# Optimization experiments

Hardware: AMD Instinct MI355X
Metric: run time of the kernel (lower is better)

## Reference

```python
import jax, jax.numpy as jnp
import numpy as np

B, S, ID = 4, 1024, 4096
R, RP, H, D = 512, 64, 32, 128  # lora_rank, rope_dim, n_heads, head_dim
EPS = 1.1920929e-07  # torch nn.RMSNorm default eps = finfo(float32).eps


def rms_norm(x, w):
    return x * jax.lax.rsqrt(jnp.mean(x * x, axis=-1, keepdims=True) + EPS) * w


def rope(x, cos_half, sin_half):
    # half/half pairing rotation (HF style)
    cos = jnp.concatenate([cos_half, cos_half], axis=-1)
    sin = jnp.concatenate([sin_half, sin_half], axis=-1)
    half = x.shape[-1] // 2
    rot = jnp.concatenate([-x[..., half:], x[..., :half]], axis=-1)
    return x * cos + rot * sin


def setup_inputs() -> dict:
    key = jax.random.key(0)
    ks = jax.random.split(key, 12)
    sc = 0.02
    x = jax.random.normal(ks[0], (B, S, ID), jnp.float32)
    # real RoPE tables, shape (S, RP//2)
    inv_freq = 1.0 / (10000.0 ** (jnp.arange(0, RP, 2, dtype=jnp.float32) / RP))
    ang = jnp.arange(S, dtype=jnp.float32)[:, None] * inv_freq[None, :]
    cos_half = jnp.cos(ang)
    sin_half = jnp.sin(ang)
    mask = jnp.zeros((S, S), jnp.float32)  # additive mask; no softmax in module so keep finite
    return {
        "x": x,
        "cos_half": cos_half,
        "sin_half": sin_half,
        "mask": mask,
        "w_dkv_kr_w": jax.random.normal(ks[1], (R + RP, ID), jnp.float32) * sc,
        "w_dkv_kr_b": jnp.zeros((R + RP,), jnp.float32),
        "kv_norm_w": jnp.ones((R,), jnp.float32),
        "w_dq_w": jax.random.normal(ks[2], (R, ID), jnp.float32) * sc,
        "w_dq_b": jnp.zeros((R,), jnp.float32),
        "q_norm_w": jnp.ones((R,), jnp.float32),
        "w_uq_w": jax.random.normal(ks[3], (H * D, R), jnp.float32) * sc,
        "w_uq_b": jnp.zeros((H * D,), jnp.float32),
        "w_qr_w": jax.random.normal(ks[4], (RP, R), jnp.float32) * sc,
        "w_qr_b": jnp.zeros((RP,), jnp.float32),
        "w_uk_w": jax.random.normal(ks[5], (H * D, R), jnp.float32) * sc,
        "w_uv_w": jax.random.normal(ks[6], (H * D, R), jnp.float32) * sc,
        "w_o_w": jax.random.normal(ks[7], (ID, H * D), jnp.float32) * sc,
        "w_o_b": jnp.zeros((ID,), jnp.float32),
        "start_pos": 0,
    }


def reference(x, cos_half, sin_half, mask, w_dkv_kr_w, w_dkv_kr_b, kv_norm_w,
              w_dq_w, w_dq_b, q_norm_w, w_uq_w, w_uq_b, w_qr_w, w_qr_b,
              w_uk_w, w_uv_w, w_o_w, w_o_b, start_pos):
    b, s, _ = x.shape
    # KV down-projection + decoupled rope key
    dkv = x @ w_dkv_kr_w.T + w_dkv_kr_b                      # (b,s,R+RP)
    c_kv = rms_norm(dkv[..., :R], kv_norm_w)                 # (b,s,R) == kv_cache[:,start:end] (start_pos=0, prefill)
    k_r = rope(dkv[..., R:], cos_half, sin_half)             # (b,s,RP) == pe_cache slice
    # Q path
    c_q = rms_norm(x @ w_dq_w.T + w_dq_b, q_norm_w)          # (b,s,R)
    q = (c_q @ w_uq_w.T + w_uq_b).reshape(b, s, H, D)        # (b,s,h,d)
    q_r = rope(c_q @ w_qr_w.T + w_qr_b, cos_half, sin_half)  # (b,s,RP)
    # weight absorption: fold w_uk into the query
    qW = jnp.einsum('bshd,hdr->bshr', q, w_uk_w.reshape(H, D, R))
    scores = jnp.einsum('bshr,btr->bsht', qW, c_kv)
    scores = scores + jnp.einsum('bsd,btd->bst', q_r, k_r)[:, :, None, :]
    scores = scores + mask[:, None, :]                       # (s,1,t) broadcast over (b,s,h,t)
    # NOTE: faithful to source -- no softmax / no scaling applied
    a_sum = jnp.einsum('bsht,btr->bshr', scores, c_kv)
    out = jnp.einsum('bshr,hdr->bshd', a_sum, w_uv_w.reshape(H, D, R))
    out = out.reshape(b, s, H * D)
    return out @ w_o_w.T + w_o_b
```

## Files before the change

### kernel.cpp

```cpp
#include <hip/hip_runtime.h>
#include <hip/hip_bf16.h>

typedef __attribute__((ext_vector_type(8))) short s8v;
typedef __attribute__((ext_vector_type(4))) float f4v;
typedef __hip_bfloat16 bf16;

#define BSZ 4
#define SEQ 1024
#define IDIM 4096
#define RNK 512
#define RPD 64
#define NH 32
#define HD 128
#define BT 4096

__device__ __forceinline__ void load_lds16(const bf16* g, bf16* l) {
  __builtin_amdgcn_global_load_lds((const __attribute__((address_space(1))) void*)g,
                                   (__attribute__((address_space(3))) void*)l, 16, 0, 0);
}

template<int OUT_BF16, int HAS_BIAS>
__global__ __launch_bounds__(512, 2) void gemm256(
    const bf16* __restrict__ A, const bf16* __restrict__ B, void* __restrict__ Cv,
    const float* __restrict__ bias, int K, int lda, int ldb, int ldc, int NXT)
{
  __shared__ bf16 As[2][256 * 64];
  __shared__ bf16 Bs[2][256 * 64];

  int nwg = gridDim.x, orig = blockIdx.x, cpx = nwg >> 3;
  int l = (orig & 7) * cpx + (orig >> 3);
  int tx = l % NXT, ty = l / NXT;
  long long rowBase = (long long)ty * 256;
  long long colBase = (long long)tx * 256;

  int tid = threadIdx.x, lane = tid & 63, wave = tid >> 6;
  int wr = wave >> 2, wc = wave & 3;
  int lrow = lane & 15, lslot = lane >> 4;
  int NT = K >> 6;

  int srow = tid >> 3, sslot = tid & 7;
  int skc = sslot ^ (srow & 7);
  int sdst = srow * 64 + sslot * 8;
  const bf16* aP0 = A + (rowBase + srow      ) * lda + (skc << 3);
  const bf16* aP1 = A + (rowBase + srow +  64) * lda + (skc << 3);
  const bf16* aP2 = A + (rowBase + srow + 128) * lda + (skc << 3);
  const bf16* aP3 = A + (rowBase + srow + 192) * lda + (skc << 3);
  const bf16* bP0 = B + (colBase + srow      ) * ldb + (skc << 3);
  const bf16* bP1 = B + (colBase + srow +  64) * ldb + (skc << 3);
  const bf16* bP2 = B + (colBase + srow + 128) * ldb + (skc << 3);
  const bf16* bP3 = B + (colBase + srow + 192) * ldb + (skc << 3);

#define SG_A(bs, dk, i) load_lds16(aP##i + (dk) * 64, &As[bs][sdst + (i) * 4096])
#define SG_B(bs, dk, i) load_lds16(bP##i + (dk) * 64, &Bs[bs][sdst + (i) * 4096])

  int offk0 = ((lslot ^ (lrow & 7)) << 3);
  int offk1 = (((4 | lslot) ^ (lrow & 7)) << 3);
  int aoff = (wr * 128 + lrow) * 64;
  int boff = (wc * 64 + lrow) * 64;

  f4v acc[8][4];
  #pragma unroll
  for (int m = 0; m < 8; ++m)
    #pragma unroll
    for (int n = 0; n < 4; ++n) acc[m][n] = {0.f, 0.f, 0.f, 0.f};

#define PHASE(BSEL, Q, STG, GATE) do {                                         \
    const bf16* Ab_ = &As[BSEL][aoff];                                         \
    s8v a00 = *(const s8v*)(Ab_ + (2*(Q))   * 1024 + offk0);                   \
    s8v a01 = *(const s8v*)(Ab_ + (2*(Q))   * 1024 + offk1);                   \
    s8v a10 = *(const s8v*)(Ab_ + (2*(Q)+1) * 1024 + offk0);                   \
    s8v a11 = *(const s8v*)(Ab_ + (2*(Q)+1) * 1024 + offk1);                   \
    if ((Q) == 0) {                                                            \
      const bf16* Bb_ = &Bs[BSEL][boff];                                       \
      _Pragma("unroll")                                                        \
      for (int n = 0; n < 4; ++n) {                                            \
        b0[n] = *(const s8v*)(Bb_ + n * 1024 + offk0);                         \
        b1[n] = *(const s8v*)(Bb_ + n * 1024 + offk1);                         \
      }                                                                        \
    }                                                                          \
    STG;                                                                       \
    if ((Q) == 0) asm volatile("s_waitcnt lgkmcnt(8)");                        \
    __builtin_amdgcn_s_barrier();                                              \
    __builtin_amdgcn_s_setprio(1);                                             \
    _Pragma("unroll")                                                          \
    for (int n = 0; n < 4; ++n)                                                \
      acc[2*(Q)][n]   = __builtin_amdgcn_mfma_f32_16x16x32_bf16(a00, b0[n], acc[2*(Q)][n], 0, 0, 0);   \
    _Pragma("unroll")                                                          \
    for (int n = 0; n < 4; ++n)                                                \
      acc[2*(Q)+1][n] = __builtin_amdgcn_mfma_f32_16x16x32_bf16(a10, b0[n], acc[2*(Q)+1][n], 0, 0, 0); \
    _Pragma("unroll")                                                          \
    for (int n = 0; n < 4; ++n)                                                \
      acc[2*(Q)][n]   = __builtin_amdgcn_mfma_f32_16x16x32_bf16(a01, b1[n], acc[2*(Q)][n], 0, 0, 0);   \
    _Pragma("unroll")                                                          \
    for (int n = 0; n < 4; ++n)                                                \
      acc[2*(Q)+1][n] = __builtin_amdgcn_mfma_f32_16x16x32_bf16(a11, b1[n], acc[2*(Q)+1][n], 0, 0, 0); \
    __builtin_amdgcn_s_setprio(0);                                             \
    GATE;                                                                      \
    __builtin_amdgcn_s_barrier();                                              \
  } while (0)

  SG_A(0, 0, 0); SG_A(0, 0, 1); SG_A(0, 0, 2); SG_A(0, 0, 3);
  SG_B(0, 0, 0); SG_B(0, 0, 1); SG_B(0, 0, 2); SG_B(0, 0, 3);
  SG_B(1, 1, 0); SG_B(1, 1, 1); SG_B(1, 1, 2); SG_B(1, 1, 3);
  asm volatile("s_waitcnt vmcnt(4)" ::: "memory");
  __builtin_amdgcn_s_barrier();

  for (int u = 0; u < NT; u += 2) {
    bool st = (u + 2 < NT);
    s8v b0[4], b1[4];
    PHASE(0, 0, { SG_A(1, 1, 0); SG_A(1, 1, 1); }, {});
    PHASE(0, 1, { SG_A(1, 1, 2); SG_A(1, 1, 3); }, {});
    PHASE(0, 2, { if (st) { SG_B(0, 2, 0); SG_B(0, 2, 1); } }, {});
    PHASE(0, 3, { if (st) { SG_B(0, 2, 2); SG_B(0, 2, 3); } },
          { if (st) asm volatile("s_waitcnt vmcnt(4)" ::: "memory");
            else    asm volatile("s_waitcnt vmcnt(0)" ::: "memory"); });
    PHASE(1, 0, { if (st) { SG_A(0, 2, 0); SG_A(0, 2, 1); } }, {});
    PHASE(1, 1, { if (st) { SG_A(0, 2, 2); SG_A(0, 2, 3); } }, {});
    PHASE(1, 2, { if (st) { SG_B(1, 3, 0); SG_B(1, 3, 1); } }, {});
    PHASE(1, 3, { if (st) { SG_B(1, 3, 2); SG_B(1, 3, 3); } },
          { if (st) asm volatile("s_waitcnt vmcnt(4)" ::: "memory"); });
    aP0 += 128; aP1 += 128; aP2 += 128; aP3 += 128;
    bP0 += 128; bP1 += 128; bP2 += 128; bP3 += 128;
  }
#undef PHASE
#undef SG_A
#undef SG_B

  float* Cf = (float*)Cv;
  bf16* Cb = (bf16*)Cv;
  int lcol = lane & 15, lr4 = (lane >> 4) * 4;
  #pragma unroll
  for (int m = 0; m < 8; ++m)
    #pragma unroll
    for (int n = 0; n < 4; ++n) {
      long long col = colBase + wc * 64 + n * 16 + lcol;
      float bv_ = HAS_BIAS ? bias[col] : 0.f;
      #pragma unroll
      for (int j = 0; j < 4; ++j) {
        long long row = rowBase + wr * 128 + m * 16 + lr4 + j;
        float v = acc[m][n][j] + bv_;
        if (OUT_BF16) Cb[row * ldc + col] = __float2bfloat16(v);
        else          Cf[row * ldc + col] = v;
      }
    }
}

template<int BM, int BN, int WTM, int WTN, int OUT_BF16, int ADD_MODE, int HAS_BIAS>
__global__ __launch_bounds__(256) void gemm_bt(
    const bf16* __restrict__ A, const bf16* __restrict__ B, void* __restrict__ Cv,
    const float* __restrict__ bias, const void* __restrict__ addend,
    int K, int lda, int ldb, int ldc, int ldadd, int nz2,
    long long sA1, long long sA2, long long sB1, long long sB2,
    long long sC1, long long sC2, long long sD1, long long sD2)
{
  constexpr int BK = 32;
  constexpr int WM = BM / WTM, WN = BN / WTN;
  constexpr int FM = WM / 16, FN = WN / 16;
  static_assert(WTM * WTN == 4, "4 waves / 256 threads");
  static_assert((BM * BK) % 2048 == 0 && (BN * BK) % 2048 == 0, "staging coverage");
  __shared__ alignas(16) bf16 As[BM * BK];
  __shared__ alignas(16) bf16 Bs[BN * BK];

  int z = blockIdx.z;
  int z1 = z / nz2, z2 = z - z1 * nz2;
  A += z1 * sA1 + z2 * sA2;
  B += z1 * sB1 + z2 * sB2;
  long long coff = z1 * sC1 + z2 * sC2;
  long long doffz = z1 * sD1 + z2 * sD2;

  int tid = threadIdx.x;
  int lane = tid & 63, wave = tid >> 6;
  int wr = wave / WTN, wc = wave % WTN;
  int rowBase = blockIdx.y * BM;
  int colBase = blockIdx.x * BN;

  f4v acc[FM][FN];
  #pragma unroll
  for (int i = 0; i < FM; ++i)
    #pragma unroll
    for (int j = 0; j < FN; ++j) acc[i][j] = {0.f, 0.f, 0.f, 0.f};

  constexpr int A_LOADS = (BM * BK) / 2048;
  constexpr int B_LOADS = (BN * BK) / 2048;
  int lrow = lane & 15;
  int rsw = (lrow >> 1) & 3;
  int lkA = ((lane >> 4) ^ rsw) * 8;

  for (int k0 = 0; k0 < K; k0 += BK) {
    #pragma unroll
    for (int i = 0; i < A_LOADS; ++i) {
      int e = tid * 8 + i * 2048;
      int r_ = e >> 5, sp_ = (e >> 3) & 3, kc_ = sp_ ^ ((r_ >> 1) & 3);
      load_lds16(A + (long long)(rowBase + r_) * lda + k0 + (kc_ << 3), &As[e]);
    }
    #pragma unroll
    for (int i = 0; i < B_LOADS; ++i) {
      int e = tid * 8 + i * 2048;
      int r_ = e >> 5, sp_ = (e >> 3) & 3, kc_ = sp_ ^ ((r_ >> 1) & 3);
      load_lds16(B + (long long)(colBase + r_) * ldb + k0 + (kc_ << 3), &Bs[e]);
    }
    __syncthreads();

    s8v av[FM], bv[FN];
    #pragma unroll
    for (int fm = 0; fm < FM; ++fm)
      av[fm] = *(const s8v*)&As[(wr * WM + fm * 16 + lrow) * BK + lkA];
    #pragma unroll
    for (int fn = 0; fn < FN; ++fn)
      bv[fn] = *(const s8v*)&Bs[(wc * WN + fn * 16 + lrow) * BK + lkA];
    #pragma unroll
    for (int fm = 0; fm < FM; ++fm)
      #pragma unroll
      for (int fn = 0; fn < FN; ++fn)
        acc[fm][fn] = __builtin_amdgcn_mfma_f32_16x16x32_bf16(av[fm], bv[fn], acc[fm][fn], 0, 0, 0);
    __syncthreads();
  }

  bf16* Cb = (bf16*)Cv;
  float* Cf = (float*)Cv;
  const float* addf = (const float*)addend;
  const bf16* addb = (const bf16*)addend;
  int lcol = lane & 15, lr4 = (lane >> 4) * 4;
  #pragma unroll
  for (int fm = 0; fm < FM; ++fm) {
    #pragma unroll
    for (int fn = 0; fn < FN; ++fn) {
      int col = colBase + wc * WN + fn * 16 + lcol;
      #pragma unroll
      for (int j = 0; j < 4; ++j) {
        int row = rowBase + wr * WM + fm * 16 + lr4 + j;
        float v = acc[fm][fn][j];
        if (HAS_BIAS) v += bias[col];
        if (ADD_MODE == 1) v += addf[doffz + (long long)row * ldadd + col];
        if (ADD_MODE == 2) v += __bfloat162float(addb[doffz + (long long)row * ldadd + col]);
        long long idx = coff + (long long)row * ldc + col;
        if (OUT_BF16) Cb[idx] = __float2bfloat16(v);
        else          Cf[idx] = v;
      }
    }
  }
}


__global__ void cast4(const float* __restrict__ in, bf16* __restrict__ out, int n4) {
  int i = blockIdx.x * 256 + threadIdx.x;
  if (i >= n4) return;
  float4 v = ((const float4*)in)[i];
  union { ushort4 u; bf16 h[4]; } o;
  o.h[0] = __float2bfloat16(v.x); o.h[1] = __float2bfloat16(v.y);
  o.h[2] = __float2bfloat16(v.z); o.h[3] = __float2bfloat16(v.w);
  ((ushort4*)out)[i] = o.u;
}

struct CastJobs {
  const float* s[8];
  bf16* d[8];
  int n4[8];
  int b0[8];
};
__global__ __launch_bounds__(256) void cast_multi(CastJobs J) {
  int blk = blockIdx.x, j = 0;
  #pragma unroll
  for (int k = 1; k < 8; ++k) if (blk >= J.b0[k]) j = k;
  int i = (blk - J.b0[j]) * 256 + threadIdx.x;
  if (i >= J.n4[j]) return;
  float4 v = ((const float4*)J.s[j])[i];
  union { ushort4 u; bf16 h[4]; } o;
  o.h[0] = __float2bfloat16(v.x); o.h[1] = __float2bfloat16(v.y);
  o.h[2] = __float2bfloat16(v.z); o.h[3] = __float2bfloat16(v.w);
  ((ushort4*)J.d[j])[i] = o.u;
}

__global__ __launch_bounds__(256) void tr_bf16(const bf16* __restrict__ in, bf16* __restrict__ out,
                                               int R, int C) {
  __shared__ bf16 t[32][33];
  long long zo = (long long)blockIdx.z * R * C;
  int c0 = blockIdx.x * 32, r0 = blockIdx.y * 32;
  int tx = threadIdx.x & 31, ty = threadIdx.x >> 5;
  #pragma unroll
  for (int i = 0; i < 32; i += 8)
    t[ty + i][tx] = in[zo + (long long)(r0 + ty + i) * C + (c0 + tx)];
  __syncthreads();
  #pragma unroll
  for (int i = 0; i < 32; i += 8)
    out[zo + (long long)(c0 + ty + i) * R + (r0 + tx)] = t[tx][ty + i];
}

__device__ __forceinline__ float block_sum256(float v) {
  #pragma unroll
  for (int o = 32; o > 0; o >>= 1) v += __shfl_xor(v, o, 64);
  __shared__ float red[4];
  int lane = threadIdx.x & 63, w = threadIdx.x >> 6;
  if (lane == 0) red[w] = v;
  __syncthreads();
  return red[0] + red[1] + red[2] + red[3];
}

__global__ __launch_bounds__(256) void rms_dkv(const float* __restrict__ dq,
    const float* __restrict__ w, const float* __restrict__ ch, const float* __restrict__ sh,
    bf16* __restrict__ ckv, bf16* __restrict__ kr) {
  int row = blockIdx.x, t = threadIdx.x;
  const float* xr = dq + (long long)row * 1088;
  float v0 = xr[t], v1 = xr[t + 256];
  float ss = block_sum256(v0 * v0 + v1 * v1);
  float sc = rsqrtf(ss * (1.0f / 512.0f) + 1.1920929e-07f);
  long long o = (long long)row * 512;
  ckv[o + t]       = __float2bfloat16(v0 * sc * w[t]);
  ckv[o + t + 256] = __float2bfloat16(v1 * sc * w[t + 256]);
  if (t < 64) {
    int s = row & (SEQ - 1);
    float a = xr[512 + t], r;
    if (t < 32) r = a * ch[s * 32 + t]      - xr[512 + t + 32] * sh[s * 32 + t];
    else        r = a * ch[s * 32 + t - 32] + xr[512 + t - 32] * sh[s * 32 + t - 32];
    kr[(long long)row * 64 + t] = __float2bfloat16(r);
  }
}

__global__ __launch_bounds__(256) void rms512(const float* __restrict__ dq,
    const float* __restrict__ w, bf16* __restrict__ out) {
  int row = blockIdx.x, t = threadIdx.x;
  const float* xr = dq + (long long)row * 1088 + 576;
  float v0 = xr[t], v1 = xr[t + 256];
  float ss = block_sum256(v0 * v0 + v1 * v1);
  float sc = rsqrtf(ss * (1.0f / 512.0f) + 1.1920929e-07f);
  long long o = (long long)row * 512;
  out[o + t]       = __float2bfloat16(v0 * sc * w[t]);
  out[o + t + 256] = __float2bfloat16(v1 * sc * w[t + 256]);
}

__global__ void rope_qr(const float* __restrict__ in, const float* __restrict__ ch,
                        const float* __restrict__ sh, bf16* __restrict__ out) {
  int row = blockIdx.x, t = threadIdx.x;
  const float* xr = in + (long long)row * 64;
  int s = row & (SEQ - 1);
  float a = xr[t], r;
  if (t < 32) r = a * ch[s * 32 + t]      - xr[t + 32] * sh[s * 32 + t];
  else        r = a * ch[s * 32 + t - 32] + xr[t - 32] * sh[s * 32 + t - 32];
  out[(long long)row * 64 + t] = __float2bfloat16(r);
}

extern "C" void kernel_launch(void* const* d_in, const int* in_sizes, int n_in,
                              void* d_out, int out_size, void* d_ws, size_t ws_size,
                              hipStream_t stream) {
  const float* x    = (const float*)d_in[0];
  const float* ch   = (const float*)d_in[1];
  const float* sh   = (const float*)d_in[2];
  const float* mask = (const float*)d_in[3];
  const float* wdkv = (const float*)d_in[4];
  const float* bdkv = (const float*)d_in[5];
  const float* kvnw = (const float*)d_in[6];
  const float* wdq  = (const float*)d_in[7];
  const float* bdq  = (const float*)d_in[8];
  const float* qnw  = (const float*)d_in[9];
  const float* wuq  = (const float*)d_in[10];
  const float* buq  = (const float*)d_in[11];
  const float* wqr  = (const float*)d_in[12];
  const float* bqr  = (const float*)d_in[13];
  const float* wuk  = (const float*)d_in[14];
  const float* wuv  = (const float*)d_in[15];
  const float* wo   = (const float*)d_in[16];
  const float* bo   = (const float*)d_in[17];
  float* out = (float*)d_out;
  (void)in_sizes; (void)n_in; (void)out_size; (void)ws_size;

  char* ws = (char*)d_ws;
  bf16* regionA = (bf16*)(ws);
  bf16* outh    = (bf16*)(ws + 33554432);
  bf16* wdkv_b  = (bf16*)(ws + 67108864);
  bf16* wdq_b   = (bf16*)(ws + 71827456);
  bf16* wuq_b   = (bf16*)(ws + 76021760);
  bf16* wqr_b   = (bf16*)(ws + 80216064);
  bf16* wuv_b   = (bf16*)(ws + 80281600);
  bf16* wuk_b   = (bf16*)(ws + 84475904);
  bf16* mask_b  = (bf16*)(ws + 88670208);
  char* regionB = ws + 90767360;
  float* dq_cat = (float*)(regionB);
  bf16* Eb      = (bf16*)(regionB);
  bf16* FT      = (bf16*)(regionB + 16777216);

  bf16* xb   = regionA;
  bf16* wo_b = regionA;

  char* ob = (char*)d_out;
  bf16* qb     = (bf16*)(ob);
  char* U      = ob + 33554432;
  bf16* ckv    = (bf16*)(U);
  bf16* kr     = (bf16*)(U + 4194304);
  bf16* ckvT   = (bf16*)(U + 4718592);
  bf16* krT    = (bf16*)(U + 8912896);
  bf16* cq     = (bf16*)(U + 9437184);
  float* qr_pre= (float*)(U + 13631488);
  bf16* qr_b   = (bf16*)(U + 14680064);
  bf16* Gm     = (bf16*)(U + 15204352);
  bf16* Mt     = (bf16*)(U + 17301504);
  bf16* base_b = (bf16*)(U + 17563648);

  float* bias_cat = qr_pre;

  long long Z = 0;

  {
    CastJobs J;
    const float* srcs[8] = {x, wdkv, wdq, wqr, mask, wuq, wuv, wuk};
    bf16* dsts[8] = {xb, wdkv_b, wdq_b, wqr_b, mask_b, wuq_b, wuv_b, wuk_b};
    int n4s[8] = {4194304, 589824, 524288, 8192, 262144, 524288, 524288, 524288};
    int accb = 0;
    for (int j = 0; j < 8; ++j) {
      J.s[j] = srcs[j]; J.d[j] = dsts[j]; J.n4[j] = n4s[j];
      J.b0[j] = accb; accb += (n4s[j] + 255) / 256;
    }
    cast_multi<<<dim3(accb), 256, 0, stream>>>(J);
  }
  hipMemcpyAsync(bias_cat, bdkv, 576 * 4, hipMemcpyDeviceToDevice, stream);
  hipMemcpyAsync(bias_cat + 576, bdq, 512 * 4, hipMemcpyDeviceToDevice, stream);

  gemm_bt<128, 64, 4, 1, 0, 0, 1><<<dim3(17, 32, 1), 256, 0, stream>>>(
      xb, wdkv_b, dq_cat, bias_cat, nullptr, 4096, 4096, 4096, 1088, 0, 1, Z,Z,Z,Z,Z,Z,Z,Z);
  rms_dkv<<<dim3(BT), 256, 0, stream>>>(dq_cat, kvnw, ch, sh, ckv, kr);
  rms512<<<dim3(BT), 256, 0, stream>>>(dq_cat, qnw, cq);
  tr_bf16<<<dim3(16, 32, 4), 256, 0, stream>>>(ckv, ckvT, 1024, 512);
  tr_bf16<<<dim3(2, 32, 4), 256, 0, stream>>>(kr, krT, 1024, 64);

  cast4<<<dim3(16384), 256, 0, stream>>>(wo, wo_b, 4194304);

  gemm256<1, 1><<<dim3(256), 512, 0, stream>>>(
      cq, wuq_b, qb, buq, 512, 512, 512, 4096, 16);

  gemm_bt<128, 64, 4, 1, 0, 0, 1><<<dim3(1, 32, 1), 256, 0, stream>>>(
      cq, wqr_b, qr_pre, bqr, nullptr, 512, 512, 512, 64, 0, 1, Z,Z,Z,Z,Z,Z,Z,Z);
  rope_qr<<<dim3(BT), 64, 0, stream>>>(qr_pre, ch, sh, qr_b);

  gemm_bt<128, 128, 2, 2, 1, 0, 0><<<dim3(4, 4, 4), 256, 0, stream>>>(
      ckvT, ckvT, Gm, nullptr, nullptr, 1024, 1024, 1024, 512, 0, 1,
      524288LL, Z, 524288LL, Z, 262144LL, Z, Z, Z);

  gemm_bt<128, 64, 4, 1, 1, 0, 0><<<dim3(1, 4, 4), 256, 0, stream>>>(
      ckvT, krT, Mt, nullptr, nullptr, 1024, 1024, 1024, 64, 0, 1,
      524288LL, Z, 65536LL, Z, 32768LL, Z, Z, Z);

  gemm_bt<128, 128, 2, 2, 1, 0, 0><<<dim3(4, 8, 4), 256, 0, stream>>>(
      mask_b, ckvT, base_b, nullptr, nullptr, 1024, 1024, 1024, 512, 0, 1,
      Z, Z, 524288LL, Z, 524288LL, Z, Z, Z);

  gemm_bt<128, 128, 2, 2, 1, 2, 0><<<dim3(4, 8, 4), 256, 0, stream>>>(
      qr_b, Mt, base_b, nullptr, base_b, 64, 64, 64, 512, 512, 1,
      65536LL, Z, 32768LL, Z, 524288LL, Z, 524288LL, Z);

  gemm256<1, 0><<<dim3(256), 512, 0, stream>>>(
      base_b, wuv_b, outh, nullptr, 512, 512, 512, 4096, 16);

  gemm_bt<128, 128, 2, 2, 1, 0, 0><<<dim3(4, 1, 128), 256, 0, stream>>>(
      wuv_b, Gm, Eb, nullptr, nullptr, 512, 512, 512, 512, 0, 32,
      Z, 65536LL, 262144LL, Z, 2097152LL, 65536LL, Z, Z);

  gemm_bt<128, 128, 2, 2, 1, 0, 0><<<dim3(1, 1, 128), 256, 0, stream>>>(
      Eb, wuk_b, FT, nullptr, nullptr, 512, 512, 512, 128, 0, 32,
      2097152LL, 65536LL, Z, 65536LL, 524288LL, 16384LL, Z, Z);

  gemm_bt<128, 128, 2, 2, 1, 2, 0><<<dim3(1, 8, 128), 256, 0, stream>>>(
      qb, FT, outh, nullptr, outh, 128, 4096, 128, 4096, 4096, 32,
      4194304LL, 128LL, 524288LL, 16384LL, 4194304LL, 128LL, 4194304LL, 128LL);

  gemm256<0, 1><<<dim3(256), 512, 0, stream>>>(
      outh, wo_b, out, bo, 4096, 4096, 4096, 4096, 16);
}
```

Baseline: 458.9 us.

## Halve K-tile depth and software-pipeline LDS fragment reads across MFMA phases

The 256x256 GEMM now stages K=32 slices instead of 64, which halves shared memory per buffer. It changes the swizzle and staging layout and prefetches the next A/B register fragments while the current MFMAs run. Launch bounds drop to one block per SIMD-pair hint so the extra prefetch registers fit. This is meant to hide LDS read latency behind matrix math, at the cost of twice as many barriers per unit of K and possibly lower occupancy.

```diff
diff --git a/kernel.cpp b/kernel.cpp
--- a/kernel.cpp
+++ b/kernel.cpp
@@ -20,12 +20,12 @@
 }
 
 template<int OUT_BF16, int HAS_BIAS>
-__global__ __launch_bounds__(512, 2) void gemm256(
+__global__ __launch_bounds__(512, 1) void gemm256(
     const bf16* __restrict__ A, const bf16* __restrict__ B, void* __restrict__ Cv,
     const float* __restrict__ bias, int K, int lda, int ldb, int ldc, int NXT)
 {
-  __shared__ bf16 As[2][256 * 64];
-  __shared__ bf16 Bs[2][256 * 64];
+  __shared__ bf16 As[2][256 * 32];
+  __shared__ bf16 Bs[2][256 * 32];
 
   int nwg = gridDim.x, orig = blockIdx.x, cpx = nwg >> 3;
   int l = (orig & 7) * cpx + (orig >> 3);
@@ -36,27 +36,29 @@
   int tid = threadIdx.x, lane = tid & 63, wave = tid >> 6;
   int wr = wave >> 2, wc = wave & 3;
   int lrow = lane & 15, lslot = lane >> 4;
-  int NT = K >> 6;
-
-  int srow = tid >> 3, sslot = tid & 7;
-  int skc = sslot ^ (srow & 7);
-  int sdst = srow * 64 + sslot * 8;
-  const bf16* aP0 = A + (rowBase + srow      ) * lda + (skc << 3);
-  const bf16* aP1 = A + (rowBase + srow +  64) * lda + (skc << 3);
-  const bf16* aP2 = A + (rowBase + srow + 128) * lda + (skc << 3);
-  const bf16* aP3 = A + (rowBase + srow + 192) * lda + (skc << 3);
-  const bf16* bP0 = B + (colBase + srow      ) * ldb + (skc << 3);
-  const bf16* bP1 = B + (colBase + srow +  64) * ldb + (skc << 3);
-  const bf16* bP2 = B + (colBase + srow + 128) * ldb + (skc << 3);
-  const bf16* bP3 = B + (colBase + srow + 192) * ldb + (skc << 3);
-
-#define SG_A(bs, dk, i) load_lds16(aP##i + (dk) * 64, &As[bs][sdst + (i) * 4096])
-#define SG_B(bs, dk, i) load_lds16(bP##i + (dk) * 64, &Bs[bs][sdst + (i) * 4096])
-
-  int offk0 = ((lslot ^ (lrow & 7)) << 3);
-  int offk1 = (((4 | lslot) ^ (lrow & 7)) << 3);
-  int aoff = (wr * 128 + lrow) * 64;
-  int boff = (wc * 64 + lrow) * 64;
+  int NT = K >> 5;
+
+  int r0 = tid >> 2, sp = tid & 3;
+  int kc0 = sp ^ ((r0 >> 1) & 3);
+  const bf16* aQ0 = A + (rowBase + r0      ) * lda + kc0 * 8;
+  const bf16* aQ1 = A + (rowBase + r0 + 128) * lda + kc0 * 8;
+  const bf16* bQ0 = B + (colBase + r0      ) * ldb + kc0 * 8;
+  const bf16* bQ1 = B + (colBase + r0 + 128) * ldb + kc0 * 8;
+  int sdst = tid * 8;
+
+#define SGA(bs, dk, h) load_lds16((h ? aQ1 : aQ0) + (dk) * 32, &As[bs][sdst + (h) * 4096])
+#define SGB(bs, dk, h) load_lds16((h ? bQ1 : bQ0) + (dk) * 32, &Bs[bs][sdst + (h) * 4096])
+
+  int kOff = (lslot ^ ((lrow >> 1) & 3)) * 8;
+  int aBase = (wr * 128 + lrow) * 32 + kOff;
+  int bBase = (wc * 64 + lrow) * 32 + kOff;
+
+#define RD_A(d0, d1, bs, m) do { \
+    d0 = *(const s8v*)&As[bs][aBase + (m) * 512]; \
+    d1 = *(const s8v*)&As[bs][aBase + ((m) + 1) * 512]; } while (0)
+#define RD_B(arr, bs) do { \
+    _Pragma("unroll") \
+    for (int n_ = 0; n_ < 4; ++n_) arr[n_] = *(const s8v*)&Bs[bs][bBase + n_ * 512]; } while (0)
 
   f4v acc[8][4];
   #pragma unroll
@@ -64,67 +66,73 @@
     #pragma unroll
     for (int n = 0; n < 4; ++n) acc[m][n] = {0.f, 0.f, 0.f, 0.f};
 
-#define PHASE(BSEL, Q, STG, GATE) do {                                         \
-    const bf16* Ab_ = &As[BSEL][aoff];                                         \
-    s8v a00 = *(const s8v*)(Ab_ + (2*(Q))   * 1024 + offk0);                   \
-    s8v a01 = *(const s8v*)(Ab_ + (2*(Q))   * 1024 + offk1);                   \
-    s8v a10 = *(const s8v*)(Ab_ + (2*(Q)+1) * 1024 + offk0);                   \
-    s8v a11 = *(const s8v*)(Ab_ + (2*(Q)+1) * 1024 + offk1);                   \
-    if ((Q) == 0) {                                                            \
-      const bf16* Bb_ = &Bs[BSEL][boff];                                       \
-      _Pragma("unroll")                                                        \
-      for (int n = 0; n < 4; ++n) {                                            \
-        b0[n] = *(const s8v*)(Bb_ + n * 1024 + offk0);                         \
-        b1[n] = *(const s8v*)(Bb_ + n * 1024 + offk1);                         \
-      }                                                                        \
-    }                                                                          \
-    STG;                                                                       \
-    if ((Q) == 0) asm volatile("s_waitcnt lgkmcnt(8)");                        \
-    __builtin_amdgcn_s_barrier();                                              \
-    __builtin_amdgcn_s_setprio(1);                                             \
-    _Pragma("unroll")                                                          \
-    for (int n = 0; n < 4; ++n)                                                \
-      acc[2*(Q)][n]   = __builtin_amdgcn_mfma_f32_16x16x32_bf16(a00, b0[n], acc[2*(Q)][n], 0, 0, 0);   \
-    _Pragma("unroll")                                                          \
-    for (int n = 0; n < 4; ++n)                                                \
-      acc[2*(Q)+1][n] = __builtin_amdgcn_mfma_f32_16x16x32_bf16(a10, b0[n], acc[2*(Q)+1][n], 0, 0, 0); \
-    _Pragma("unroll")                                                          \
-    for (int n = 0; n < 4; ++n)                                                \
-      acc[2*(Q)][n]   = __builtin_amdgcn_mfma_f32_16x16x32_bf16(a01, b1[n], acc[2*(Q)][n], 0, 0, 0);   \
-    _Pragma("unroll")                                                          \
-    for (int n = 0; n < 4; ++n)                                                \
-      acc[2*(Q)+1][n] = __builtin_amdgcn_mfma_f32_16x16x32_bf16(a11, b1[n], acc[2*(Q)+1][n], 0, 0, 0); \
-    __builtin_amdgcn_s_setprio(0);                                             \
-    GATE;                                                                      \
-    __builtin_amdgcn_s_barrier();                                              \
-  } while (0)
-
-  SG_A(0, 0, 0); SG_A(0, 0, 1); SG_A(0, 0, 2); SG_A(0, 0, 3);
-  SG_B(0, 0, 0); SG_B(0, 0, 1); SG_B(0, 0, 2); SG_B(0, 0, 3);
-  SG_B(1, 1, 0); SG_B(1, 1, 1); SG_B(1, 1, 2); SG_B(1, 1, 3);
-  asm volatile("s_waitcnt vmcnt(4)" ::: "memory");
+#define MMP(mp, A0, A1, BB) do { \
+    __builtin_amdgcn_s_setprio(1); \
+    _Pragma("unroll") \
+    for (int n_ = 0; n_ < 4; ++n_) { \
+      acc[mp][n_]       = __builtin_amdgcn_mfma_f32_16x16x32_bf16(A0, BB[n_], acc[mp][n_], 0, 0, 0); \
+      acc[(mp) + 1][n_] = __builtin_amdgcn_mfma_f32_16x16x32_bf16(A1, BB[n_], acc[(mp) + 1][n_], 0, 0, 0); \
+    } \
+    __builtin_amdgcn_s_setprio(0); } while (0)
+
+  s8v aX0, aX1, aY0, aY1;
+  s8v bX[4], bY[4];
+
+  SGA(0, 0, 0); SGA(0, 0, 1);
+  SGB(0, 0, 0); SGB(0, 0, 1);
+  SGB(1, 1, 0); SGB(1, 1, 1);
+  asm volatile("s_waitcnt vmcnt(2)" ::: "memory");
   __builtin_amdgcn_s_barrier();
+  RD_B(bX, 0);
+  RD_A(aX0, aX1, 0, 0);
 
   for (int u = 0; u < NT; u += 2) {
     bool st = (u + 2 < NT);
-    s8v b0[4], b1[4];
-    PHASE(0, 0, { SG_A(1, 1, 0); SG_A(1, 1, 1); }, {});
-    PHASE(0, 1, { SG_A(1, 1, 2); SG_A(1, 1, 3); }, {});
-    PHASE(0, 2, { if (st) { SG_B(0, 2, 0); SG_B(0, 2, 1); } }, {});
-    PHASE(0, 3, { if (st) { SG_B(0, 2, 2); SG_B(0, 2, 3); } },
-          { if (st) asm volatile("s_waitcnt vmcnt(4)" ::: "memory");
-            else    asm volatile("s_waitcnt vmcnt(0)" ::: "memory"); });
-    PHASE(1, 0, { if (st) { SG_A(0, 2, 0); SG_A(0, 2, 1); } }, {});
-    PHASE(1, 1, { if (st) { SG_A(0, 2, 2); SG_A(0, 2, 3); } }, {});
-    PHASE(1, 2, { if (st) { SG_B(1, 3, 0); SG_B(1, 3, 1); } }, {});
-    PHASE(1, 3, { if (st) { SG_B(1, 3, 2); SG_B(1, 3, 3); } },
-          { if (st) asm volatile("s_waitcnt vmcnt(4)" ::: "memory"); });
-    aP0 += 128; aP1 += 128; aP2 += 128; aP3 += 128;
-    bP0 += 128; bP1 += 128; bP2 += 128; bP3 += 128;
+    RD_A(aY0, aY1, 0, 2);
+    SGA(1, 1, 0);
+    MMP(0, aX0, aX1, bX);
+    __builtin_amdgcn_s_barrier();
+    RD_A(aX0, aX1, 0, 4);
+    SGA(1, 1, 1);
+    MMP(2, aY0, aY1, bX);
+    __builtin_amdgcn_s_barrier();
+    RD_A(aY0, aY1, 0, 6);
+    if (st) SGB(0, 2, 0);
+    MMP(4, aX0, aX1, bX);
+    if (st) asm volatile("s_waitcnt vmcnt(1)");
+    else    asm volatile("s_waitcnt vmcnt(0)");
+    __builtin_amdgcn_s_barrier();
+    RD_B(bY, 1);
+    RD_A(aX0, aX1, 1, 0);
+    if (st) SGB(0, 2, 1);
+    MMP(6, aY0, aY1, bX);
+    __builtin_amdgcn_s_barrier();
+    RD_A(aY0, aY1, 1, 2);
+    if (st) SGA(0, 2, 0);
+    MMP(0, aX0, aX1, bY);
+    __builtin_amdgcn_s_barrier();
+    RD_A(aX0, aX1, 1, 4);
+    if (st) SGA(0, 2, 1);
+    MMP(2, aY0, aY1, bY);
+    __builtin_amdgcn_s_barrier();
+    RD_A(aY0, aY1, 1, 6);
+    if (st) SGB(1, 3, 0);
+    MMP(4, aX0, aX1, bY);
+    if (st) asm volatile("s_waitcnt vmcnt(1)");
+    else    asm volatile("s_waitcnt vmcnt(0)");
+    __builtin_amdgcn_s_barrier();
+    if (st) { RD_B(bX, 0); RD_A(aX0, aX1, 0, 0); }
+    if (st) SGB(1, 3, 1);
+    MMP(6, aY0, aY1, bY);
+    __builtin_amdgcn_s_barrier();
+
+    aQ0 += 64; aQ1 += 64; bQ0 += 64; bQ1 += 64;
   }
-#undef PHASE
-#undef SG_A
-#undef SG_B
+#undef SGA
+#undef SGB
+#undef RD_A
+#undef RD_B
+#undef MMP
 
   float* Cf = (float*)Cv;
   bf16* Cb = (bf16*)Cv;
```

Measured after the change: 473.5 us. +3.2%, slower.
